# Kernel optimization log

Measured on AMD Instinct MI355X. Metric: run time of the kernel, lower is better.

Reference implementation:

```python
import jax, jax.numpy as jnp
import numpy as np

B, S, HID = 2, 2048, 1024
H, D = 16, HID // 16  # heads, head_dim
ROPE_BASE = 10000.0


def setup_inputs() -> dict:
    key = jax.random.key(0)
    k1, k2, k3, k4 = jax.random.split(key, 4)
    scale = 1.0 / np.sqrt(HID)
    return {
        "hidden_states": jax.random.normal(k1, (B, S, HID), dtype=jnp.float32),
        "attention_mask": jnp.zeros((B, 1, 1, S), dtype=jnp.float32),
        "Wq": jax.random.normal(k2, (HID, HID), dtype=jnp.float32) * scale,
        "Wk": jax.random.normal(k3, (HID, HID), dtype=jnp.float32) * scale,
        "Wv": jax.random.normal(k4, (HID, HID), dtype=jnp.float32) * scale,
    }


def _rope_cos_sin(seq_len, dim, dtype):
    inv_freq = 1.0 / (ROPE_BASE ** (jnp.arange(0, dim, 2, dtype=jnp.float32) / dim))
    freqs = jnp.arange(seq_len, dtype=jnp.float32)[:, None] * inv_freq[None, :]  # (S, D/2)
    emb = jnp.concatenate([freqs, freqs], axis=-1)  # (S, D)
    return jnp.cos(emb).astype(dtype), jnp.sin(emb).astype(dtype)


def _rotate_half(x):
    x1, x2 = jnp.split(x, 2, axis=-1)
    return jnp.concatenate([-x2, x1], axis=-1)


def reference(hidden_states, attention_mask, Wq, Wk, Wv):
    b, s, _ = hidden_states.shape
    # QKV projections (no bias), split into heads: (b, H, s, D)
    def proj(W):
        return jnp.einsum('bse,de->bsd', hidden_states, W).reshape(b, s, H, D).transpose(0, 2, 1, 3)
    q, k, v = proj(Wq), proj(Wk), proj(Wv)
    # Rotary embedding on q, k over sequence positions
    cos, sin = _rope_cos_sin(s, D, hidden_states.dtype)  # (s, D)
    cos = cos[None, None]  # (1,1,s,D)
    sin = sin[None, None]
    q = q * cos + _rotate_half(q) * sin
    k = k * cos + _rotate_half(k) * sin
    # Scaled dot-product attention with additive mask
    scores = jnp.einsum('bhqd,bhkd->bhqk', q, k) / jnp.sqrt(jnp.asarray(D, hidden_states.dtype))
    scores = scores + attention_mask
    probs = jax.nn.softmax(scores, axis=-1)  # dropout p=0 (eval) -> identity
    ctx = jnp.einsum('bhqk,bhkd->bhqd', probs, v)
    return ctx.transpose(0, 2, 1, 3).reshape(b, s, H * D)
```

## Files before the change

### kernel.cpp

```cpp
#include <hip/hip_runtime.h>
#include <stdint.h>

typedef unsigned short u16;
typedef short bf16x8 __attribute__((ext_vector_type(8)));
typedef float f32x4 __attribute__((ext_vector_type(4)));

#define S_ 2048
#define HID_ 1024
#define H_ 16
#define D_ 64

#define LOG2E 1.4426950408889634f
#define SCALE_LOG2 0.18033688011112042f
#define MAXC_LOG2 11.541560327111707f

__device__ __forceinline__ u16 f2bf(float f) {
  uint32_t x = __builtin_bit_cast(uint32_t, f);
  uint32_t r = (x + 0x7fffu + ((x >> 16) & 1u)) >> 16;
  return (u16)r;
}
__device__ __forceinline__ uint32_t packbf2(float a, float b) {
  return (uint32_t)f2bf(a) | ((uint32_t)f2bf(b) << 16);
}
__device__ __forceinline__ uint32_t permpack(float a, float b) {
  return __builtin_amdgcn_perm(__builtin_bit_cast(uint32_t, b),
                               __builtin_bit_cast(uint32_t, a), 0x07060302u);
}

__device__ __forceinline__ void gl2lds16(const void* g, void* l) {
  __builtin_amdgcn_global_load_lds(
      (const __attribute__((address_space(1))) unsigned int*)g,
      (__attribute__((address_space(3))) unsigned int*)l, 16, 0, 0);
}

#define NX_ (1 << 20)
#define NW_ (1 << 18)
#define NROPE_ 65536
__global__ void prep_kernel(const float* __restrict__ X, const float* __restrict__ Wq,
                            const float* __restrict__ Wk, const float* __restrict__ Wv,
                            const float* __restrict__ mask, u16* __restrict__ Xb,
                            u16* __restrict__ Wqb, u16* __restrict__ Wkb,
                            u16* __restrict__ Wvb, float* __restrict__ cos_t,
                            float* __restrict__ sin_t, float* __restrict__ mask2) {
  int i = blockIdx.x * 256 + threadIdx.x;
  if (i < NX_ + 3 * NW_) {
    const float* src;
    u16* dst;
    int off;
    if (i < NX_) {
      src = X; dst = Xb; off = i;
    } else if (i < NX_ + NW_) {
      src = Wq; dst = Wqb; off = i - NX_;
    } else if (i < NX_ + 2 * NW_) {
      src = Wk; dst = Wkb; off = i - NX_ - NW_;
    } else {
      src = Wv; dst = Wvb; off = i - NX_ - 2 * NW_;
    }
    float4 v = ((const float4*)src)[off];
    uint2 packed;
    packed.x = packbf2(v.x, v.y);
    packed.y = packbf2(v.z, v.w);
    ((uint2*)dst)[off] = packed;
  } else if (i < NX_ + 3 * NW_ + NROPE_) {
    int t = i - (NX_ + 3 * NW_);
    int s = t >> 5, j = t & 31;
    float invf = powf(10000.0f, -(float)j * (1.0f / 32.0f));
    float ang = (float)s * invf;
    cos_t[t] = cosf(ang);
    sin_t[t] = sinf(ang);
  } else {
    int t = i - (NX_ + 3 * NW_ + NROPE_);
    mask2[t] = fmaf(mask[t], LOG2E, -MAXC_LOG2);
  }
}

__global__ __launch_bounds__(256) void qkv_gemm_kernel(
    const u16* __restrict__ X, const u16* __restrict__ Wq, const u16* __restrict__ Wk,
    const u16* __restrict__ Wv, const float* __restrict__ cos_t,
    const float* __restrict__ sin_t, u16* __restrict__ Q, u16* __restrict__ K,
    u16* __restrict__ Vt) {
  __shared__ char smem[65536];
  int tid = threadIdx.x;
  int lane = tid & 63, wave = tid >> 6;
  int wm = wave >> 1, wn = wave & 1;
  int quad = lane >> 4, l16 = lane & 15;
  int which = blockIdx.x >> 3;
  int nbase = (blockIdx.x & 7) * 128;
  int mbase = blockIdx.y * 128;
  const u16* W = (which == 0) ? Wq : (which == 1) ? Wk : Wv;

#pragma unroll
  for (int it = 0; it < 4; ++it) {
    int i = it * 256 + tid;
    int r = i >> 3, gs = i & 7, gsrc = gs ^ (r & 7);
    gl2lds16(X + (size_t)(mbase + r) * HID_ + gsrc * 8, smem + i * 16);
    gl2lds16(W + (size_t)(nbase + r) * HID_ + gsrc * 8, smem + 32768 + i * 16);
  }

  f32x4 acc[4][4] = {};

  for (int kk = 0; kk < 16; ++kk) {
    char* As = smem + (kk & 1) * 16384;
    char* Bs = smem + 32768 + (kk & 1) * 16384;
    __syncthreads();

    if (kk < 15) {
      int k0n = (kk + 1) * 64;
      char* An = smem + ((kk + 1) & 1) * 16384;
      char* Bn = smem + 32768 + ((kk + 1) & 1) * 16384;
#pragma unroll
      for (int it = 0; it < 4; ++it) {
        int i = it * 256 + tid;
        int r = i >> 3, gs = i & 7, gsrc = gs ^ (r & 7);
        gl2lds16(X + (size_t)(mbase + r) * HID_ + k0n + gsrc * 8, An + i * 16);
        gl2lds16(W + (size_t)(nbase + r) * HID_ + k0n + gsrc * 8, Bn + i * 16);
      }
    }

#pragma unroll
    for (int kh = 0; kh < 2; ++kh) {
      bf16x8 afrag[4], bfrag[4];
#pragma unroll
      for (int i4 = 0; i4 < 4; ++i4) {
        int r = wm * 64 + i4 * 16 + l16;
        int L = r * 8 + ((kh * 4 + quad) ^ (r & 7));
        afrag[i4] = *(const bf16x8*)(As + L * 16);
      }
#pragma unroll
      for (int j4 = 0; j4 < 4; ++j4) {
        int r = wn * 64 + j4 * 16 + l16;
        int L = r * 8 + ((kh * 4 + quad) ^ (r & 7));
        bfrag[j4] = *(const bf16x8*)(Bs + L * 16);
      }
      if (which == 2) {
#pragma unroll
        for (int i4 = 0; i4 < 4; ++i4)
#pragma unroll
          for (int j4 = 0; j4 < 4; ++j4)
            acc[i4][j4] = __builtin_amdgcn_mfma_f32_16x16x32_bf16(afrag[i4], bfrag[j4],
                                                                  acc[i4][j4], 0, 0, 0);
      } else {
#pragma unroll
        for (int i4 = 0; i4 < 4; ++i4)
#pragma unroll
          for (int j4 = 0; j4 < 4; ++j4)
            acc[i4][j4] = __builtin_amdgcn_mfma_f32_16x16x32_bf16(bfrag[j4], afrag[i4],
                                                                  acc[i4][j4], 0, 0, 0);
      }
    }
  }

  if (which == 2) {
#pragma unroll
    for (int i4 = 0; i4 < 4; ++i4)
#pragma unroll
      for (int j4 = 0; j4 < 4; ++j4) {
        int m = mbase + wm * 64 + i4 * 16 + quad * 4;
        int n = nbase + wn * 64 + j4 * 16 + l16;
        int b = m >> 11, s0 = m & 2047;
        int h = n >> 6, d = n & 63;
        uint2 pk;
        pk.x = packbf2(acc[i4][j4][0], acc[i4][j4][1]);
        pk.y = packbf2(acc[i4][j4][2], acc[i4][j4][3]);
        *(uint2*)(Vt + (((size_t)(b * H_ + h)) * D_ + d) * S_ + s0) = pk;
      }
  } else {
    u16* dst = (which == 0) ? Q : K;
#pragma unroll
    for (int i4 = 0; i4 < 4; ++i4)
#pragma unroll
      for (int j4 = 0; j4 < 2; ++j4) {
        int m = mbase + wm * 64 + i4 * 16 + l16;
        int n1 = nbase + wn * 64 + j4 * 16 + quad * 4;
        int b = m >> 11, s = m & 2047;
        int h = n1 >> 6, d1 = n1 & 63;
        float4 c4 = *(const float4*)(cos_t + s * 32 + d1);
        float4 s4 = *(const float4*)(sin_t + s * 32 + d1);
        float y1[4], y2[4];
#pragma unroll
        for (int r = 0; r < 4; ++r) {
          float cr = ((const float*)&c4)[r], sr = ((const float*)&s4)[r];
          float x1 = acc[i4][j4][r], x2 = acc[i4][j4 + 2][r];
          y1[r] = x1 * cr - x2 * sr;
          y2[r] = x2 * cr + x1 * sr;
        }
        size_t base = ((size_t)(b * H_ + h) * S_ + s) * D_;
        uint2 p1, p2;
        p1.x = packbf2(y1[0], y1[1]);
        p1.y = packbf2(y1[2], y1[3]);
        p2.x = packbf2(y2[0], y2[1]);
        p2.y = packbf2(y2[2], y2[3]);
        *(uint2*)(dst + base + d1) = p1;
        *(uint2*)(dst + base + d1 + 32) = p2;
      }
  }
}

__device__ __forceinline__ void pv_step(const char* Pr, const char* Vp, int quad, int l16,
                                        const bf16x8& ones, f32x4* o, f32x4& lacc) {
  bf16x8 p[2];
#pragma unroll
  for (int kh = 0; kh < 2; ++kh) {
    int c0 = kh * 8 + quad * 2;
    union { uint2 u[2]; bf16x8 v; } cv;
    cv.u[0] = *(const uint2*)(Pr + l16 * 128 + ((c0) ^ l16) * 8);
    cv.u[1] = *(const uint2*)(Pr + l16 * 128 + ((c0 + 1) ^ l16) * 8);
    p[kh] = cv.v;
  }
  lacc = __builtin_amdgcn_mfma_f32_16x16x32_bf16(p[0], ones, lacc, 0, 0, 0);
  lacc = __builtin_amdgcn_mfma_f32_16x16x32_bf16(p[1], ones, lacc, 0, 0, 0);
#pragma unroll
  for (int jd = 0; jd < 4; ++jd) {
    int r = jd * 16 + l16;
#pragma unroll
    for (int kh = 0; kh < 2; ++kh) {
      int L = r * 8 + ((kh * 4 + quad) ^ (r & 7));
      bf16x8 vf = *(const bf16x8*)(Vp + L * 16);
      o[jd] = __builtin_amdgcn_mfma_f32_16x16x32_bf16(p[kh], vf, o[jd], 0, 0, 0);
    }
  }
}

__global__ __launch_bounds__(512, 4) void flash_kernel(
    const u16* __restrict__ Q, const u16* __restrict__ K, const u16* __restrict__ Vt,
    const float* __restrict__ mask2, float* __restrict__ out) {
  __shared__ char smem[65536];
  int tid = threadIdx.x, wave = tid >> 6;
  int lane = tid & 63;
  int quad = lane >> 4, l16 = lane & 15;
  int bh = blockIdx.y, b = bh >> 4, h = bh & 15;
  int qbase = blockIdx.x * 128;
  int qw = qbase + wave * 16;
  char* Pw = smem + 49152 + wave * 2048;
  const float* m2row = mask2 + b * S_;
  const u16* Kbase = K + (size_t)bh * S_ * D_;
  const u16* Vbase = Vt + (size_t)bh * D_ * S_;

  bf16x8 qfrag[2];
  {
    const u16* qp = Q + ((size_t)bh * S_ + qw + l16) * D_ + quad * 8;
    qfrag[0] = *(const bf16x8*)qp;
    qfrag[1] = *(const bf16x8*)(qp + 32);
  }
  bf16x8 ones;
#pragma unroll
  for (int j = 0; j < 8; ++j) ones[j] = (short)0x3f80;

  f32x4 o[4] = {};
  f32x4 lacc = {};

  {
    int i = tid;
    int r = i >> 3, gs = i & 7, gsrc = gs ^ (r & 7);
    gl2lds16(Kbase + (size_t)r * D_ + gsrc * 8, smem + i * 16);
    gl2lds16(Vbase + (size_t)r * S_ + gsrc * 8, smem + 8192 + i * 16);
  }
  float4 mv[4];
#pragma unroll
  for (int jt = 0; jt < 4; ++jt) mv[jt] = *(const float4*)(m2row + jt * 16 + quad * 4);

  for (int kt = 0; kt < 32; ++kt) {
    char* Ks = smem + (kt % 3) * 16384;
    __syncthreads();

    if (kt < 31) {
      char* Kn = smem + ((kt + 1) % 3) * 16384;
      char* Vn = Kn + 8192;
      int nb = (kt + 1) * 64;
      int i = tid;
      int r = i >> 3, gs = i & 7, gsrc = gs ^ (r & 7);
      gl2lds16(Kbase + (size_t)(nb + r) * D_ + gsrc * 8, Kn + i * 16);
      gl2lds16(Vbase + (size_t)r * S_ + nb + gsrc * 8, Vn + i * 16);
    }

    if (kt > 0) {
      const char* Vp = smem + ((kt - 1) % 3) * 16384 + 8192;
      pv_step(Pw, Vp, quad, l16, ones, o, lacc);
    }

    f32x4 s[4] = {};
#pragma unroll
    for (int jt = 0; jt < 4; ++jt) {
      int r = jt * 16 + l16;
#pragma unroll
      for (int kh = 0; kh < 2; ++kh) {
        int L = r * 8 + ((kh * 4 + quad) ^ (r & 7));
        bf16x8 kf = *(const bf16x8*)(Ks + L * 16);
        s[jt] = __builtin_amdgcn_mfma_f32_16x16x32_bf16(kf, qfrag[kh], s[jt], 0, 0, 0);
      }
    }

#pragma unroll
    for (int jt = 0; jt < 4; ++jt) {
      float pf[4];
#pragma unroll
      for (int r = 0; r < 4; ++r) {
        float mvr = ((const float*)&mv[jt])[r];
        pf[r] = __builtin_amdgcn_exp2f(fmaf(s[jt][r], SCALE_LOG2, mvr));
      }
      uint2 pk;
      pk.x = permpack(pf[0], pf[1]);
      pk.y = permpack(pf[2], pf[3]);
      int chunk = (jt * 4 + quad) ^ l16;
      *(uint2*)(Pw + l16 * 128 + chunk * 8) = pk;
    }

    if (kt < 31) {
#pragma unroll
      for (int jt = 0; jt < 4; ++jt)
        mv[jt] = *(const float4*)(m2row + (kt + 1) * 64 + jt * 16 + quad * 4);
    }
  }

  pv_step(Pw, smem + 16384 + 8192, quad, l16, ones, o, lacc);

  float inv[4];
#pragma unroll
  for (int r = 0; r < 4; ++r) inv[r] = 1.0f / lacc[r];
#pragma unroll
  for (int jd = 0; jd < 4; ++jd) {
#pragma unroll
    for (int r = 0; r < 4; ++r) {
      int d = jd * 16 + l16;
      int q = qw + quad * 4 + r;
      out[(((size_t)b * S_ + q) * H_ + h) * D_ + d] = o[jd][r] * inv[r];
    }
  }
}

extern "C" void kernel_launch(void* const* d_in, const int* in_sizes, int n_in,
                              void* d_out, int out_size, void* d_ws, size_t ws_size,
                              hipStream_t stream) {
  const float* hid = (const float*)d_in[0];
  const float* mask = (const float*)d_in[1];
  const float* Wq = (const float*)d_in[2];
  const float* Wk = (const float*)d_in[3];
  const float* Wv = (const float*)d_in[4];
  float* out = (float*)d_out;
  char* ws = (char*)d_ws;

  u16* Xbf = (u16*)ws;
  u16* Wqb = (u16*)(ws + (8u << 20));
  u16* Wkb = (u16*)(ws + (10u << 20));
  u16* Wvb = (u16*)(ws + (12u << 20));
  u16* Qb = (u16*)(ws + (14u << 20));
  u16* Kb = (u16*)(ws + (22u << 20));
  u16* Vtb = (u16*)(ws + (30u << 20));
  float* cos_t = (float*)(ws + (38u << 20));
  float* sin_t = (float*)(ws + (38u << 20) + (256u << 10));
  float* mask2 = (float*)(ws + (38u << 20) + (512u << 10));

  prep_kernel<<<7440, 256, 0, stream>>>(hid, Wq, Wk, Wv, mask, Xbf, Wqb, Wkb, Wvb,
                                        cos_t, sin_t, mask2);
  qkv_gemm_kernel<<<dim3(24, 32), 256, 0, stream>>>(Xbf, Wqb, Wkb, Wvb, cos_t, sin_t,
                                                    Qb, Kb, Vtb);
  flash_kernel<<<dim3(16, 32), 512, 0, stream>>>(Qb, Kb, Vtb, mask2, out);
}
```

Before: 171.0 us.

## Switch flash attention to 32x32x16 MFMA with 32-row query tiles per wave

Rewrites the attention kernel to use 32x32x16 bf16 MFMA instructions, with each wave owning 32 query rows instead of 16. The block shrinks from 512 to 256 threads, so each thread loads two K/V chunks per tile. The P tile swizzle, mask fragment loads and output write pattern are reworked to fit the new accumulator layout. The aim is fewer MFMA issues and more reuse of each K/V LDS read, at the cost of higher register pressure and fewer waves per block.

```diff
diff --git a/kernel.cpp b/kernel.cpp
--- a/kernel.cpp
+++ b/kernel.cpp
@@ -4,6 +4,7 @@
 typedef unsigned short u16;
 typedef short bf16x8 __attribute__((ext_vector_type(8)));
 typedef float f32x4 __attribute__((ext_vector_type(4)));
+typedef float f32x16 __attribute__((ext_vector_type(16)));
 
 #define S_ 2048
 #define HID_ 1024
@@ -196,68 +197,68 @@
   }
 }
 
-__device__ __forceinline__ void pv_step(const char* Pr, const char* Vp, int quad, int l16,
-                                        const bf16x8& ones, f32x4* o, f32x4& lacc) {
-  bf16x8 p[2];
-#pragma unroll
-  for (int kh = 0; kh < 2; ++kh) {
-    int c0 = kh * 8 + quad * 2;
-    union { uint2 u[2]; bf16x8 v; } cv;
-    cv.u[0] = *(const uint2*)(Pr + l16 * 128 + ((c0) ^ l16) * 8);
-    cv.u[1] = *(const uint2*)(Pr + l16 * 128 + ((c0 + 1) ^ l16) * 8);
-    p[kh] = cv.v;
-  }
-  lacc = __builtin_amdgcn_mfma_f32_16x16x32_bf16(p[0], ones, lacc, 0, 0, 0);
-  lacc = __builtin_amdgcn_mfma_f32_16x16x32_bf16(p[1], ones, lacc, 0, 0, 0);
-#pragma unroll
-  for (int jd = 0; jd < 4; ++jd) {
-    int r = jd * 16 + l16;
-#pragma unroll
-    for (int kh = 0; kh < 2; ++kh) {
-      int L = r * 8 + ((kh * 4 + quad) ^ (r & 7));
-      bf16x8 vf = *(const bf16x8*)(Vp + L * 16);
-      o[jd] = __builtin_amdgcn_mfma_f32_16x16x32_bf16(p[kh], vf, o[jd], 0, 0, 0);
-    }
-  }
-}
-
-__global__ __launch_bounds__(512, 4) void flash_kernel(
+__device__ __forceinline__ void pv32(const char* Pw, const char* Vp, int q31, int hf,
+                                     const bf16x8& ones, f32x16& o0, f32x16& o1,
+                                     f32x16& lacc) {
+  int l7 = q31 & 7;
+  bf16x8 pf[4];
+#pragma unroll
+  for (int c = 0; c < 4; ++c) {
+    int ch = (2 * c + hf) ^ l7;
+    pf[c] = *(const bf16x8*)(Pw + q31 * 128 + ch * 16);
+  }
+#pragma unroll
+  for (int c = 0; c < 4; ++c)
+    lacc = __builtin_amdgcn_mfma_f32_32x32x16_bf16(pf[c], ones, lacc, 0, 0, 0);
+#pragma unroll
+  for (int c = 0; c < 4; ++c) {
+    int ch = (2 * c + hf) ^ l7;
+    bf16x8 v0 = *(const bf16x8*)(Vp + q31 * 128 + ch * 16);
+    bf16x8 v1 = *(const bf16x8*)(Vp + (32 + q31) * 128 + ch * 16);
+    o0 = __builtin_amdgcn_mfma_f32_32x32x16_bf16(pf[c], v0, o0, 0, 0, 0);
+    o1 = __builtin_amdgcn_mfma_f32_32x32x16_bf16(pf[c], v1, o1, 0, 0, 0);
+  }
+}
+
+__global__ __launch_bounds__(256, 2) void flash_kernel(
     const u16* __restrict__ Q, const u16* __restrict__ K, const u16* __restrict__ Vt,
     const float* __restrict__ mask2, float* __restrict__ out) {
   __shared__ char smem[65536];
   int tid = threadIdx.x, wave = tid >> 6;
   int lane = tid & 63;
-  int quad = lane >> 4, l16 = lane & 15;
-  int bh = blockIdx.y, b = bh >> 4, h = bh & 15;
-  int qbase = blockIdx.x * 128;
-  int qw = qbase + wave * 16;
-  char* Pw = smem + 49152 + wave * 2048;
+  int q31 = lane & 31, hf = lane >> 5, l7 = lane & 7;
+  int bh = blockIdx.y, b = bh >> 4, hh = bh & 15;
+  int qw = blockIdx.x * 128 + wave * 32;
+  char* Pw = smem + 49152 + wave * 4096;
   const float* m2row = mask2 + b * S_;
   const u16* Kbase = K + (size_t)bh * S_ * D_;
   const u16* Vbase = Vt + (size_t)bh * D_ * S_;
 
-  bf16x8 qfrag[2];
+  bf16x8 qfrag[4];
   {
-    const u16* qp = Q + ((size_t)bh * S_ + qw + l16) * D_ + quad * 8;
-    qfrag[0] = *(const bf16x8*)qp;
-    qfrag[1] = *(const bf16x8*)(qp + 32);
+    const u16* qp = Q + ((size_t)bh * S_ + qw + q31) * D_ + 8 * hf;
+#pragma unroll
+    for (int c = 0; c < 4; ++c) qfrag[c] = *(const bf16x8*)(qp + 16 * c);
   }
   bf16x8 ones;
 #pragma unroll
   for (int j = 0; j < 8; ++j) ones[j] = (short)0x3f80;
 
-  f32x4 o[4] = {};
-  f32x4 lacc = {};
-
-  {
-    int i = tid;
+  f32x16 o0 = {}, o1 = {}, lacc = {};
+
+#pragma unroll
+  for (int it = 0; it < 2; ++it) {
+    int i = it * 256 + tid;
     int r = i >> 3, gs = i & 7, gsrc = gs ^ (r & 7);
     gl2lds16(Kbase + (size_t)r * D_ + gsrc * 8, smem + i * 16);
     gl2lds16(Vbase + (size_t)r * S_ + gsrc * 8, smem + 8192 + i * 16);
   }
-  float4 mv[4];
-#pragma unroll
-  for (int jt = 0; jt < 4; ++jt) mv[jt] = *(const float4*)(m2row + jt * 16 + quad * 4);
+  float4 mvt[8];
+#pragma unroll
+  for (int kb = 0; kb < 2; ++kb)
+#pragma unroll
+    for (int g = 0; g < 4; ++g)
+      mvt[kb * 4 + g] = *(const float4*)(m2row + kb * 32 + g * 8 + hf * 4);
 
   for (int kt = 0; kt < 32; ++kt) {
     char* Ks = smem + (kt % 3) * 16384;
@@ -267,65 +268,69 @@
       char* Kn = smem + ((kt + 1) % 3) * 16384;
       char* Vn = Kn + 8192;
       int nb = (kt + 1) * 64;
-      int i = tid;
-      int r = i >> 3, gs = i & 7, gsrc = gs ^ (r & 7);
-      gl2lds16(Kbase + (size_t)(nb + r) * D_ + gsrc * 8, Kn + i * 16);
-      gl2lds16(Vbase + (size_t)r * S_ + nb + gsrc * 8, Vn + i * 16);
-    }
-
-    if (kt > 0) {
-      const char* Vp = smem + ((kt - 1) % 3) * 16384 + 8192;
-      pv_step(Pw, Vp, quad, l16, ones, o, lacc);
-    }
-
-    f32x4 s[4] = {};
-#pragma unroll
-    for (int jt = 0; jt < 4; ++jt) {
-      int r = jt * 16 + l16;
-#pragma unroll
-      for (int kh = 0; kh < 2; ++kh) {
-        int L = r * 8 + ((kh * 4 + quad) ^ (r & 7));
-        bf16x8 kf = *(const bf16x8*)(Ks + L * 16);
-        s[jt] = __builtin_amdgcn_mfma_f32_16x16x32_bf16(kf, qfrag[kh], s[jt], 0, 0, 0);
-      }
-    }
-
-#pragma unroll
-    for (int jt = 0; jt < 4; ++jt) {
-      float pf[4];
-#pragma unroll
-      for (int r = 0; r < 4; ++r) {
-        float mvr = ((const float*)&mv[jt])[r];
-        pf[r] = __builtin_amdgcn_exp2f(fmaf(s[jt][r], SCALE_LOG2, mvr));
-      }
-      uint2 pk;
-      pk.x = permpack(pf[0], pf[1]);
-      pk.y = permpack(pf[2], pf[3]);
-      int chunk = (jt * 4 + quad) ^ l16;
-      *(uint2*)(Pw + l16 * 128 + chunk * 8) = pk;
+#pragma unroll
+      for (int it = 0; it < 2; ++it) {
+        int i = it * 256 + tid;
+        int r = i >> 3, gs = i & 7, gsrc = gs ^ (r & 7);
+        gl2lds16(Kbase + (size_t)(nb + r) * D_ + gsrc * 8, Kn + i * 16);
+        gl2lds16(Vbase + (size_t)r * S_ + nb + gsrc * 8, Vn + i * 16);
+      }
+    }
+
+    if (kt > 0) pv32(Pw, smem + ((kt + 2) % 3) * 16384 + 8192, q31, hf, ones, o0, o1, lacc);
+
+    f32x16 s0 = {}, s1 = {};
+#pragma unroll
+    for (int c = 0; c < 4; ++c) {
+      int ch = (2 * c + hf) ^ l7;
+      bf16x8 k0 = *(const bf16x8*)(Ks + q31 * 128 + ch * 16);
+      bf16x8 k1 = *(const bf16x8*)(Ks + (32 + q31) * 128 + ch * 16);
+      s0 = __builtin_amdgcn_mfma_f32_32x32x16_bf16(k0, qfrag[c], s0, 0, 0, 0);
+      s1 = __builtin_amdgcn_mfma_f32_32x32x16_bf16(k1, qfrag[c], s1, 0, 0, 0);
+    }
+
+#pragma unroll
+    for (int kb = 0; kb < 2; ++kb) {
+#pragma unroll
+      for (int g = 0; g < 4; ++g) {
+        float pf4[4];
+#pragma unroll
+        for (int r0 = 0; r0 < 4; ++r0) {
+          float sv = kb ? s1[g * 4 + r0] : s0[g * 4 + r0];
+          pf4[r0] = __builtin_amdgcn_exp2f(
+              fmaf(sv, SCALE_LOG2, ((const float*)&mvt[kb * 4 + g])[r0]));
+        }
+        uint2 pk;
+        pk.x = permpack(pf4[0], pf4[1]);
+        pk.y = permpack(pf4[2], pf4[3]);
+        int chunk8 = (8 * kb + 2 * g + hf) ^ (2 * l7);
+        *(uint2*)(Pw + q31 * 128 + chunk8 * 8) = pk;
+      }
     }
 
     if (kt < 31) {
 #pragma unroll
-      for (int jt = 0; jt < 4; ++jt)
-        mv[jt] = *(const float4*)(m2row + (kt + 1) * 64 + jt * 16 + quad * 4);
-    }
-  }
-
-  pv_step(Pw, smem + 16384 + 8192, quad, l16, ones, o, lacc);
-
-  float inv[4];
-#pragma unroll
-  for (int r = 0; r < 4; ++r) inv[r] = 1.0f / lacc[r];
-#pragma unroll
-  for (int jd = 0; jd < 4; ++jd) {
-#pragma unroll
-    for (int r = 0; r < 4; ++r) {
-      int d = jd * 16 + l16;
-      int q = qw + quad * 4 + r;
-      out[(((size_t)b * S_ + q) * H_ + h) * D_ + d] = o[jd][r] * inv[r];
-    }
-  }
+      for (int kb = 0; kb < 2; ++kb)
+#pragma unroll
+        for (int g = 0; g < 4; ++g)
+          mvt[kb * 4 + g] =
+              *(const float4*)(m2row + (kt + 1) * 64 + kb * 32 + g * 8 + hf * 4);
+    }
+  }
+
+  pv32(Pw, smem + 16384 + 8192, q31, hf, ones, o0, o1, lacc);
+
+#pragma unroll
+  for (int g = 0; g < 4; ++g)
+#pragma unroll
+    for (int r0 = 0; r0 < 4; ++r0) {
+      int reg = g * 4 + r0;
+      int q = qw + r0 + 8 * g + 4 * hf;
+      float invl = 1.0f / lacc[reg];
+      size_t base = (((size_t)b * S_ + q) * H_ + hh) * D_;
+      out[base + q31] = o0[reg] * invl;
+      out[base + 32 + q31] = o1[reg] * invl;
+    }
 }
 
 extern "C" void kernel_launch(void* const* d_in, const int* in_sizes, int n_in,
@@ -354,5 +359,5 @@
                                         cos_t, sin_t, mask2);
   qkv_gemm_kernel<<<dim3(24, 32), 256, 0, stream>>>(Xbf, Wqb, Wkb, Wvb, cos_t, sin_t,
                                                     Qb, Kb, Vtb);
-  flash_kernel<<<dim3(16, 32), 512, 0, stream>>>(Qb, Kb, Vtb, mask2, out);
-}
+  flash_kernel<<<dim3(16, 32), 256, 0, stream>>>(Qb, Kb, Vtb, mask2, out);
+}
```

Result: no change. 172.6 us (+0.9%).
